# Kernel optimization log

Measured on AMD Instinct MI355X. Metric: run time of the kernel, lower is better.

The kernel has to match this reference:

```python
import jax, jax.numpy as jnp
import numpy as np

EMBED_DIM = 1024
B, S = 8, 2048


def setup_inputs() -> dict:
    key = jax.random.key(0)
    ks = jax.random.split(key, 9)
    d = EMBED_DIM
    scale = 1.0 / np.sqrt(d)
    return {
        "x": jax.random.normal(ks[0], (B, S, d), dtype=jnp.float32),
        "Wq": jax.random.normal(ks[1], (d, d), dtype=jnp.float32) * scale,
        "bq": jnp.zeros((d,), dtype=jnp.float32),
        "Wk": jax.random.normal(ks[2], (d, d), dtype=jnp.float32) * scale,
        "bk": jnp.zeros((d,), dtype=jnp.float32),
        "Wv": jax.random.normal(ks[3], (d, d), dtype=jnp.float32) * scale,
        "bv": jnp.zeros((d,), dtype=jnp.float32),
        "ln_gamma": jnp.ones((d,), dtype=jnp.float32),
        "ln_beta": jnp.zeros((d,), dtype=jnp.float32),
    }


def _layernorm(x, gamma, beta, eps=1e-5):
    mu = jnp.mean(x, axis=-1, keepdims=True)
    var = jnp.var(x, axis=-1, keepdims=True)
    return (x - mu) * jax.lax.rsqrt(var + eps) * gamma + beta


def reference(x, Wq, bq, Wk, bk, Wv, bv, ln_gamma, ln_beta):
    # Pre-LN single-head self-attention with residual.
    # Dropout is identity (eval mode) for a deterministic reference.
    residual = x
    xn = _layernorm(x, ln_gamma, ln_beta)
    Q = jnp.einsum('bsd,de->bse', xn, Wq.T) + bq  # torch Linear: x @ W^T + b
    K = jnp.einsum('bsd,de->bse', xn, Wk.T) + bk
    V = jnp.einsum('bsd,de->bse', xn, Wv.T) + bv
    scores = jnp.einsum('bqd,bkd->bqk', Q, K) / jnp.sqrt(jnp.float32(EMBED_DIM))
    attention_weights = jax.nn.softmax(scores, axis=-1)  # [B, S, S]
    attention_output = jnp.einsum('bqk,bkd->bqd', attention_weights, V)
    output = residual + attention_output
    return (output, attention_weights)
```

## Files before the change

kernel.cpp:

```cpp
#include <hip/hip_runtime.h>

#define EMBED 1024
#define SEQ 2048
#define BATCH 8

typedef __bf16 bf16;
typedef bf16 bf16x4 __attribute__((ext_vector_type(4)));
typedef bf16 bf16x8 __attribute__((ext_vector_type(8)));
typedef float f32x4 __attribute__((ext_vector_type(4)));

__device__ __forceinline__ void async_copy16(const bf16* g, bf16* l) {
  __builtin_amdgcn_global_load_lds(
      (const __attribute__((address_space(1))) unsigned int*)g,
      (__attribute__((address_space(3))) unsigned int*)l, 16, 0, 0);
}

template <int KDEPTH, int LDA, int LDB>
__device__ __forceinline__ void gemm_core(const bf16* __restrict__ Ab,
                                          const bf16* __restrict__ Bb,
                                          bf16* lds, f32x4 (&acc)[8][4]) {
  const int tid = (int)threadIdx.x;
  const int lane = tid & 63;
  const int wid = tid >> 6;
  const int wm = wid >> 2, wn = wid & 3;
  const int c = lane & 15, g = lane >> 4;
  const int sx = c & 7;
  constexpr int NT = KDEPTH / 64;

  auto stage_B = [&](int h, int t) {
    bf16* dst = lds + (t & 1) * 32768 + 16384 + h * 8192;
    const int k0 = t * 64;
    const bf16* src = Bb + (size_t)(h * 128) * LDB + k0;
#pragma unroll
    for (int r = 0; r < 2; ++r) {
      int idx = r * 512 + tid;
      int row = idx >> 3, slot = idx & 7;
      async_copy16(src + (size_t)row * LDB + ((slot ^ (row & 7)) * 8), dst + idx * 8);
    }
  };
  auto stage_A = [&](int q, int t) {
    bf16* dst = lds + (t & 1) * 32768 + q * 4096;
    const int k0 = t * 64;
    int rib = tid >> 3, slot = tid & 7;
    int grow = q * 32 + (rib & 31) + (rib >> 5) * 128;
    async_copy16(Ab + (size_t)grow * LDA + k0 + ((slot ^ (rib & 7)) * 8), dst + tid * 8);
  };

  stage_B(0, 0); stage_B(1, 0);
  stage_A(0, 0); stage_A(1, 0); stage_A(2, 0); stage_A(3, 0);
  asm volatile("s_waitcnt vmcnt(2)" ::: "memory");
  __builtin_amdgcn_s_barrier();
  __builtin_amdgcn_sched_barrier(0);

  const int boffb = (wn * 64 + c) * 64;
  const int arowb = (wm * 32 + c) * 64;

  for (int t = 0; t < NT; ++t) {
    const bf16* bufA = lds + (t & 1) * 32768;
    const bf16* bufB = bufA + 16384;
    const int nxt = t + 1;
    const bool more = nxt < NT;
    bf16x8 bfr[4][2];
#pragma unroll
    for (int p = 0; p < 4; ++p) {
      bf16x8 afr[2][2];
#pragma unroll
      for (int mm = 0; mm < 2; ++mm)
#pragma unroll
        for (int ks = 0; ks < 2; ++ks)
          afr[mm][ks] = *reinterpret_cast<const bf16x8*>(
              bufA + p * 4096 + arowb + mm * 1024 + (((ks * 4 + g) ^ sx) * 8));
      if (p == 0) {
#pragma unroll
        for (int ni = 0; ni < 4; ++ni)
#pragma unroll
          for (int ks = 0; ks < 2; ++ks)
            bfr[ni][ks] = *reinterpret_cast<const bf16x8*>(
                bufB + boffb + ni * 1024 + (((ks * 4 + g) ^ sx) * 8));
      }
      if (more) {
        if (p == 0) stage_B(0, nxt);
        else if (p == 1) stage_B(1, nxt);
        else if (p == 2) { stage_A(0, nxt); stage_A(1, nxt); }
        else { stage_A(2, nxt); stage_A(3, nxt); }
      }
      __builtin_amdgcn_s_barrier();
      asm volatile("s_waitcnt lgkmcnt(0)" ::: "memory");
      __builtin_amdgcn_sched_barrier(0);
      __builtin_amdgcn_s_setprio(1);
#pragma unroll
      for (int mm = 0; mm < 2; ++mm)
#pragma unroll
        for (int ni = 0; ni < 4; ++ni)
#pragma unroll
          for (int ks = 0; ks < 2; ++ks)
            acc[p * 2 + mm][ni] = __builtin_amdgcn_mfma_f32_16x16x32_bf16(
                afr[mm][ks], bfr[ni][ks], acc[p * 2 + mm][ni], 0, 0, 0);
      __builtin_amdgcn_s_setprio(0);
      __builtin_amdgcn_sched_barrier(0);
      if (p == 1) {
        if (more) asm volatile("s_waitcnt vmcnt(4)" ::: "memory");
        else      asm volatile("s_waitcnt vmcnt(0)" ::: "memory");
      }
      if (p == 3) {
        if (more) asm volatile("s_waitcnt vmcnt(2)" ::: "memory");
        else      asm volatile("s_waitcnt vmcnt(0)" ::: "memory");
      }
      __builtin_amdgcn_s_barrier();
    }
  }
}

__global__ __launch_bounds__(256) void k_pre(const float* __restrict__ x,
                                             const float* __restrict__ gamma,
                                             const float* __restrict__ beta,
                                             const float* __restrict__ wq,
                                             const float* __restrict__ wk,
                                             const float* __restrict__ wv,
                                             bf16* __restrict__ xn,
                                             bf16* __restrict__ wall) {
  const int bid = (int)blockIdx.x;
  const int tid = (int)threadIdx.x;
  if (bid >= BATCH * SEQ) {
    int i4 = (bid - BATCH * SEQ) * 256 + tid;
    int m = i4 >> 18;
    int loc = i4 & 262143;
    const float* src = (m == 0) ? wq : (m == 1) ? wk : wv;
    float4 v = reinterpret_cast<const float4*>(src)[loc];
    bf16x4 o;
    o[0] = (bf16)v.x; o[1] = (bf16)v.y; o[2] = (bf16)v.z; o[3] = (bf16)v.w;
    reinterpret_cast<bf16x4*>(wall)[i4] = o;
    return;
  }
  const int row = bid;
  const float4 v = reinterpret_cast<const float4*>(x + (size_t)row * EMBED)[tid];
  float s = v.x + v.y + v.z + v.w;
  float q = v.x * v.x + v.y * v.y + v.z * v.z + v.w * v.w;
#pragma unroll
  for (int off = 1; off < 64; off <<= 1) {
    s += __shfl_xor(s, off);
    q += __shfl_xor(q, off);
  }
  __shared__ float ls[4], lq[4];
  int w = tid >> 6;
  if ((tid & 63) == 0) { ls[w] = s; lq[w] = q; }
  __syncthreads();
  s = ls[0] + ls[1] + ls[2] + ls[3];
  q = lq[0] + lq[1] + lq[2] + lq[3];
  float mean = s * (1.0f / EMBED);
  float var = q * (1.0f / EMBED) - mean * mean;
  float rstd = rsqrtf(var + 1e-5f);
  float4 gm = reinterpret_cast<const float4*>(gamma)[tid];
  float4 b = reinterpret_cast<const float4*>(beta)[tid];
  bf16x4 o;
  o[0] = (bf16)((v.x - mean) * rstd * gm.x + b.x);
  o[1] = (bf16)((v.y - mean) * rstd * gm.y + b.y);
  o[2] = (bf16)((v.z - mean) * rstd * gm.z + b.z);
  o[3] = (bf16)((v.w - mean) * rstd * gm.w + b.w);
  reinterpret_cast<bf16x4*>(xn + (size_t)row * EMBED)[tid] = o;
}

__global__ __launch_bounds__(512) void k_qkv256(const bf16* __restrict__ xn,
                                                const bf16* __restrict__ wall,
                                                const float* __restrict__ bq,
                                                const float* __restrict__ bk,
                                                const float* __restrict__ bv,
                                                bf16* __restrict__ qbuf,
                                                bf16* __restrict__ kbuf,
                                                bf16* __restrict__ vt) {
  extern __shared__ bf16 smem[];
  const int h = (int)blockIdx.x;
  const int xcd = h & 7, pos = h >> 3;
  const int z = pos >> 5;
  const int mtile = xcd * 8 + ((pos >> 2) & 7);
  const int ntile = pos & 3;
  const int tid = (int)threadIdx.x, lane = tid & 63, wid = tid >> 6;
  const int wm = wid >> 2, wn = wid & 3;
  const int cc = lane & 15, g = lane >> 4;
  const bf16* Ab = xn + (size_t)(mtile * 256) * EMBED;
  const bf16* Bb = wall + (size_t)z * EMBED * EMBED + (size_t)(ntile * 256) * EMBED;
  f32x4 acc[8][4];
#pragma unroll
  for (int i = 0; i < 8; ++i)
#pragma unroll
    for (int j = 0; j < 4; ++j) acc[i][j] = (f32x4){0.f, 0.f, 0.f, 0.f};
  gemm_core<EMBED, EMBED, EMBED>(Ab, Bb, smem, acc);

  const int c0 = ntile * 256 + wn * 64;
  const int r0 = mtile * 256 + wm * 128;
  if (z < 2) {
    bf16* o = z ? kbuf : qbuf;
    const float* bias = z ? bk : bq;
#pragma unroll
    for (int mi = 0; mi < 8; ++mi)
#pragma unroll
      for (int ni = 0; ni < 4; ++ni) {
        int col = c0 + ni * 16 + cc;
        float bb = bias[col];
#pragma unroll
        for (int j = 0; j < 4; ++j)
          o[(size_t)(r0 + mi * 16 + g * 4 + j) * EMBED + col] = (bf16)(acc[mi][ni][j] + bb);
      }
  } else {
#pragma unroll
    for (int mi = 0; mi < 8; ++mi) {
      int srow = r0 + mi * 16 + g * 4;
      int b = srow >> 11, sl = srow & (SEQ - 1);
#pragma unroll
      for (int ni = 0; ni < 4; ++ni) {
        int col = c0 + ni * 16 + cc;
        float bb = bv[col];
        bf16x4 pk;
#pragma unroll
        for (int j = 0; j < 4; ++j) pk[j] = (bf16)(acc[mi][ni][j] + bb);
        *reinterpret_cast<bf16x4*>(vt + (size_t)b * EMBED * SEQ + (size_t)col * SEQ + sl) = pk;
      }
    }
  }
}

__global__ __launch_bounds__(512) void k_scores256(const bf16* __restrict__ qm,
                                                   const bf16* __restrict__ km,
                                                   bf16* __restrict__ wbf,
                                                   float* __restrict__ partial) {
  extern __shared__ bf16 smem[];
  const int h = (int)blockIdx.x;
  const int bb = h & 7, pos = h >> 3;
  const int mtile = pos >> 3, ntile = pos & 7;
  const int tid = (int)threadIdx.x, lane = tid & 63, wid = tid >> 6;
  const int wm = wid >> 2, wn = wid & 3;
  const int cc = lane & 15, g = lane >> 4;
  const bf16* Ab = qm + (size_t)bb * SEQ * EMBED + (size_t)(mtile * 256) * EMBED;
  const bf16* Bb = km + (size_t)bb * SEQ * EMBED + (size_t)(ntile * 256) * EMBED;
  f32x4 acc[8][4];
#pragma unroll
  for (int i = 0; i < 8; ++i)
#pragma unroll
    for (int j = 0; j < 4; ++j) acc[i][j] = (f32x4){0.f, 0.f, 0.f, 0.f};
  gemm_core<EMBED, EMBED, EMBED>(Ab, Bb, smem, acc);

  float* red = (float*)smem;
  const int c0 = ntile * 256 + wn * 64;
#pragma unroll
  for (int mi = 0; mi < 8; ++mi) {
#pragma unroll
    for (int j = 0; j < 4; ++j) {
      int lrow = wm * 128 + mi * 16 + g * 4 + j;
      size_t grow = (size_t)bb * SEQ + mtile * 256 + lrow;
      float s = 0.f;
#pragma unroll
      for (int ni = 0; ni < 4; ++ni) {
        float e = __expf(acc[mi][ni][j] * 0.03125f);
        wbf[grow * SEQ + c0 + ni * 16 + cc] = (bf16)e;
        s += e;
      }
      s += __shfl_xor(s, 1);
      s += __shfl_xor(s, 2);
      s += __shfl_xor(s, 4);
      s += __shfl_xor(s, 8);
      if (cc == 0) red[lrow * 4 + wn] = s;
    }
  }
  __syncthreads();
  if (tid < 256) {
    float l = red[tid * 4 + 0] + red[tid * 4 + 1] + red[tid * 4 + 2] + red[tid * 4 + 3];
    partial[((size_t)bb * SEQ + mtile * 256 + tid) * 8 + ntile] = l;
  }
}

__global__ __launch_bounds__(256) void k_rowsum(const float* __restrict__ partial,
                                                float* __restrict__ rinv) {
  int row = blockIdx.x * 256 + threadIdx.x;
  const float* p = partial + (size_t)row * 8;
  float l = 0.f;
#pragma unroll
  for (int i = 0; i < 8; ++i) l += p[i];
  rinv[row] = 1.0f / l;
}

__global__ __launch_bounds__(512) void k_pv256(const bf16* __restrict__ wbf,
                                               const bf16* __restrict__ vt,
                                               const float* __restrict__ rinv,
                                               const float* __restrict__ xin,
                                               float* __restrict__ outp) {
  extern __shared__ bf16 smem[];
  const int h = (int)blockIdx.x;
  const int bb = h & 7, pos = h >> 3;
  const int mtile = pos >> 2, ntile = pos & 3;
  const int tid = (int)threadIdx.x, lane = tid & 63, wid = tid >> 6;
  const int wm = wid >> 2, wn = wid & 3;
  const int cc = lane & 15, g = lane >> 4;
  const bf16* Ab = wbf + (size_t)bb * SEQ * SEQ + (size_t)(mtile * 256) * SEQ;
  const bf16* Bb = vt + (size_t)bb * EMBED * SEQ + (size_t)(ntile * 256) * SEQ;
  f32x4 acc[8][4];
#pragma unroll
  for (int i = 0; i < 8; ++i)
#pragma unroll
    for (int j = 0; j < 4; ++j) acc[i][j] = (f32x4){0.f, 0.f, 0.f, 0.f};
  gemm_core<SEQ, SEQ, SEQ>(Ab, Bb, smem, acc);

  const int c0 = ntile * 256 + wn * 64;
#pragma unroll
  for (int mi = 0; mi < 8; ++mi) {
#pragma unroll
    for (int j = 0; j < 4; ++j) {
      size_t grow = (size_t)bb * SEQ + mtile * 256 + wm * 128 + mi * 16 + g * 4 + j;
      float ri = rinv[grow];
      size_t base = grow * EMBED;
#pragma unroll
      for (int ni = 0; ni < 4; ++ni) {
        size_t off = base + c0 + ni * 16 + cc;
        outp[off] = xin[off] + acc[mi][ni][j] * ri;
      }
    }
  }
}

__global__ __launch_bounds__(256) void k_norm_bf(const bf16* __restrict__ wbf,
                                                 const float* __restrict__ rinv,
                                                 float* __restrict__ attn) {
  size_t i8 = (size_t)blockIdx.x * 256 + threadIdx.x;
  int row = (int)(i8 >> 8);
  float ri = rinv[row];
  bf16x8 v = reinterpret_cast<const bf16x8*>(wbf)[i8];
  float4 lo, hi;
  lo.x = (float)v[0] * ri; lo.y = (float)v[1] * ri;
  lo.z = (float)v[2] * ri; lo.w = (float)v[3] * ri;
  hi.x = (float)v[4] * ri; hi.y = (float)v[5] * ri;
  hi.z = (float)v[6] * ri; hi.w = (float)v[7] * ri;
  reinterpret_cast<float4*>(attn)[i8 * 2] = lo;
  reinterpret_cast<float4*>(attn)[i8 * 2 + 1] = hi;
}

extern "C" void kernel_launch(void* const* d_in, const int* in_sizes, int n_in,
                              void* d_out, int out_size, void* d_ws, size_t ws_size,
                              hipStream_t stream) {
  const float* x = (const float*)d_in[0];
  const float* Wq = (const float*)d_in[1];
  const float* bq = (const float*)d_in[2];
  const float* Wk = (const float*)d_in[3];
  const float* bk = (const float*)d_in[4];
  const float* Wv = (const float*)d_in[5];
  const float* bv = (const float*)d_in[6];
  const float* gamma = (const float*)d_in[7];
  const float* beta = (const float*)d_in[8];

  float* out = (float*)d_out;
  float* attn = out + (size_t)BATCH * SEQ * EMBED;

  bf16* qbuf = (bf16*)d_out;
  bf16* kbuf = qbuf + (size_t)BATCH * SEQ * EMBED;

  bf16* xn = (bf16*)d_ws;
  bf16* wall = xn + (size_t)BATCH * SEQ * EMBED;
  bf16* wbf = (bf16*)d_ws;
  bf16* vt = (bf16*)d_ws + (size_t)BATCH * SEQ * SEQ;
  float* partial = (float*)((char*)d_ws + 100663296ull);
  float* rinv = (float*)((char*)d_ws + 100663296ull + 524288ull);

  hipFuncSetAttribute((const void*)k_qkv256, hipFuncAttributeMaxDynamicSharedMemorySize, 131072);
  hipFuncSetAttribute((const void*)k_scores256, hipFuncAttributeMaxDynamicSharedMemorySize, 131072);
  hipFuncSetAttribute((const void*)k_pv256, hipFuncAttributeMaxDynamicSharedMemorySize, 131072);

  k_pre<<<BATCH * SEQ + 3072, 256, 0, stream>>>(x, gamma, beta, Wq, Wk, Wv, xn, wall);
  k_qkv256<<<768, 512, 131072, stream>>>(xn, wall, bq, bk, bv, qbuf, kbuf, vt);
  k_scores256<<<512, 512, 131072, stream>>>(qbuf, kbuf, wbf, partial);
  k_rowsum<<<64, 256, 0, stream>>>(partial, rinv);
  k_pv256<<<256, 512, 131072, stream>>>(wbf, vt, rinv, x, out);
  k_norm_bf<<<16384, 256, 0, stream>>>(wbf, rinv, attn);
}
```

Measured before the change: 298.0 us.

## Fuse attention-weight normalization into PV GEMM main loop

Removes the separate normalization kernel that converts exp-scores to fp32 attention weights. Each PV block now does a slice of that conversion inside the GEMM k-loop through a callback, and the vmcnt waits are adjusted to account for the extra outstanding memory operations. This saves one launch and hides the memory-bound conversion behind MFMA work. The cost is extra memory traffic competing with GEMM tile loads, plus more register pressure in the pipelined loop.

```diff
diff --git a/kernel.cpp b/kernel.cpp
--- a/kernel.cpp
+++ b/kernel.cpp
@@ -15,10 +15,11 @@
       (__attribute__((address_space(3))) unsigned int*)l, 16, 0, 0);
 }
 
-template <int KDEPTH, int LDA, int LDB>
+template <int KDEPTH, int LDA, int LDB, int E, class ExtraF>
 __device__ __forceinline__ void gemm_core(const bf16* __restrict__ Ab,
                                           const bf16* __restrict__ Bb,
-                                          bf16* lds, f32x4 (&acc)[8][4]) {
+                                          bf16* lds, f32x4 (&acc)[8][4],
+                                          ExtraF&& extra) {
   const int tid = (int)threadIdx.x;
   const int lane = tid & 63;
   const int wid = tid >> 6;
@@ -99,17 +100,35 @@
       __builtin_amdgcn_s_setprio(0);
       __builtin_amdgcn_sched_barrier(0);
       if (p == 1) {
-        if (more) asm volatile("s_waitcnt vmcnt(4)" ::: "memory");
-        else      asm volatile("s_waitcnt vmcnt(0)" ::: "memory");
+        if (more) {
+          if constexpr (E > 0) {
+            if (t == 0)
+              asm volatile("s_waitcnt vmcnt(4)" ::: "memory");
+            else
+              asm volatile("s_waitcnt vmcnt(%0)" ::"i"(4 + E) : "memory");
+          } else {
+            asm volatile("s_waitcnt vmcnt(4)" ::: "memory");
+          }
+        } else {
+          asm volatile("s_waitcnt vmcnt(0)" ::: "memory");
+        }
       }
       if (p == 3) {
-        if (more) asm volatile("s_waitcnt vmcnt(2)" ::: "memory");
-        else      asm volatile("s_waitcnt vmcnt(0)" ::: "memory");
+        extra(t);
+        __builtin_amdgcn_sched_barrier(0);
+        if (more)
+          asm volatile("s_waitcnt vmcnt(%0)" ::"i"(2 + E) : "memory");
+        else
+          asm volatile("s_waitcnt vmcnt(0)" ::: "memory");
       }
       __builtin_amdgcn_s_barrier();
     }
   }
 }
+
+struct NoExtra {
+  __device__ void operator()(int) const {}
+};
 
 __global__ __launch_bounds__(256) void k_pre(const float* __restrict__ x,
                                              const float* __restrict__ gamma,
@@ -184,7 +203,7 @@
   for (int i = 0; i < 8; ++i)
 #pragma unroll
     for (int j = 0; j < 4; ++j) acc[i][j] = (f32x4){0.f, 0.f, 0.f, 0.f};
-  gemm_core<EMBED, EMBED, EMBED>(Ab, Bb, smem, acc);
+  gemm_core<EMBED, EMBED, EMBED, 0>(Ab, Bb, smem, acc, NoExtra{});
 
   const int c0 = ntile * 256 + wn * 64;
   const int r0 = mtile * 256 + wm * 128;
@@ -237,7 +256,7 @@
   for (int i = 0; i < 8; ++i)
 #pragma unroll
     for (int j = 0; j < 4; ++j) acc[i][j] = (f32x4){0.f, 0.f, 0.f, 0.f};
-  gemm_core<EMBED, EMBED, EMBED>(Ab, Bb, smem, acc);
+  gemm_core<EMBED, EMBED, EMBED, 0>(Ab, Bb, smem, acc, NoExtra{});
 
   float* red = (float*)smem;
   const int c0 = ntile * 256 + wn * 64;
@@ -282,7 +301,8 @@
                                                const bf16* __restrict__ vt,
                                                const float* __restrict__ rinv,
                                                const float* __restrict__ xin,
-                                               float* __restrict__ outp) {
+                                               float* __restrict__ outp,
+                                               float* __restrict__ attn) {
   extern __shared__ bf16 smem[];
   const int h = (int)blockIdx.x;
   const int bb = h & 7, pos = h >> 3;
@@ -292,12 +312,28 @@
   const int cc = lane & 15, g = lane >> 4;
   const bf16* Ab = wbf + (size_t)bb * SEQ * SEQ + (size_t)(mtile * 256) * SEQ;
   const bf16* Bb = vt + (size_t)bb * EMBED * SEQ + (size_t)(ntile * 256) * SEQ;
+  const size_t nbase = (size_t)h * 16384 + tid;
   f32x4 acc[8][4];
 #pragma unroll
   for (int i = 0; i < 8; ++i)
 #pragma unroll
     for (int j = 0; j < 4; ++j) acc[i][j] = (f32x4){0.f, 0.f, 0.f, 0.f};
-  gemm_core<SEQ, SEQ, SEQ>(Ab, Bb, smem, acc);
+
+  auto norm_unit = [&](int t) {
+    size_t c = nbase + (size_t)t * 512;
+    int row = (int)(c >> 8);
+    float ri = rinv[row];
+    bf16x8 v = reinterpret_cast<const bf16x8*>(wbf)[c];
+    float4 lo, hi;
+    lo.x = (float)v[0] * ri; lo.y = (float)v[1] * ri;
+    lo.z = (float)v[2] * ri; lo.w = (float)v[3] * ri;
+    hi.x = (float)v[4] * ri; hi.y = (float)v[5] * ri;
+    hi.z = (float)v[6] * ri; hi.w = (float)v[7] * ri;
+    reinterpret_cast<float4*>(attn)[c * 2] = lo;
+    reinterpret_cast<float4*>(attn)[c * 2 + 1] = hi;
+  };
+
+  gemm_core<SEQ, SEQ, SEQ, 4>(Ab, Bb, smem, acc, norm_unit);
 
   const int c0 = ntile * 256 + wn * 64;
 #pragma unroll
@@ -314,22 +350,6 @@
       }
     }
   }
-}
-
-__global__ __launch_bounds__(256) void k_norm_bf(const bf16* __restrict__ wbf,
-                                                 const float* __restrict__ rinv,
-                                                 float* __restrict__ attn) {
-  size_t i8 = (size_t)blockIdx.x * 256 + threadIdx.x;
-  int row = (int)(i8 >> 8);
-  float ri = rinv[row];
-  bf16x8 v = reinterpret_cast<const bf16x8*>(wbf)[i8];
-  float4 lo, hi;
-  lo.x = (float)v[0] * ri; lo.y = (float)v[1] * ri;
-  lo.z = (float)v[2] * ri; lo.w = (float)v[3] * ri;
-  hi.x = (float)v[4] * ri; hi.y = (float)v[5] * ri;
-  hi.z = (float)v[6] * ri; hi.w = (float)v[7] * ri;
-  reinterpret_cast<float4*>(attn)[i8 * 2] = lo;
-  reinterpret_cast<float4*>(attn)[i8 * 2 + 1] = hi;
 }
 
 extern "C" void kernel_launch(void* const* d_in, const int* in_sizes, int n_in,
@@ -366,6 +386,5 @@
   k_qkv256<<<768, 512, 131072, stream>>>(xn, wall, bq, bk, bv, qbuf, kbuf, vt);
   k_scores256<<<512, 512, 131072, stream>>>(qbuf, kbuf, wbf, partial);
   k_rowsum<<<64, 256, 0, stream>>>(partial, rinv);
-  k_pv256<<<256, 512, 131072, stream>>>(wbf, vt, rinv, x, out);
-  k_norm_bf<<<16384, 256, 0, stream>>>(wbf, rinv, attn);
-}
+  k_pv256<<<256, 512, 131072, stream>>>(wbf, vt, rinv, x, out, attn);
+}
```

Result: no change. 300.7 us (+0.9%).
